# Optimization experiments

Measured on AMD Instinct MI355X. Metric: run time of the kernel, lower is better.

## Reference

```python
import jax, jax.numpy as jnp
import numpy as np
import math

N_EMBD = 1024
HIDDEN = 4 * N_EMBD
N_EXPERTS = 8
TOP_K = 2
B, T = 4, 2048


def new_gelu(x):
    c = math.sqrt(2.0 / math.pi)
    return 0.5 * x * (1.0 + jnp.tanh(c * (x + 0.044715 * x * x * x)))


def setup_inputs() -> dict:
    key = jax.random.key(0)
    ks = jax.random.split(key, 10)
    s = 0.02
    return {
        "x": jax.random.normal(ks[0], (B, T, N_EMBD), dtype=jnp.float32),
        # shared expert (1 shared expert)
        "Wfc_s": jax.random.normal(ks[1], (N_EMBD, HIDDEN), dtype=jnp.float32) * s,
        "bfc_s": jnp.zeros((HIDDEN,), dtype=jnp.float32),
        "Wproj_s": jax.random.normal(ks[2], (HIDDEN, N_EMBD), dtype=jnp.float32) * s,
        "bproj_s": jnp.zeros((N_EMBD,), dtype=jnp.float32),
        # router (no bias)
        "Wr": jax.random.normal(ks[3], (N_EMBD, N_EXPERTS), dtype=jnp.float32) * s,
        # routed experts, stacked on leading expert dim
        "Wfc": jax.random.normal(ks[4], (N_EXPERTS, N_EMBD, HIDDEN), dtype=jnp.float32) * s,
        "bfc": jnp.zeros((N_EXPERTS, HIDDEN), dtype=jnp.float32),
        "Wproj": jax.random.normal(ks[5], (N_EXPERTS, HIDDEN, N_EMBD), dtype=jnp.float32) * s,
        "bproj": jnp.zeros((N_EXPERTS, N_EMBD), dtype=jnp.float32),
    }


def _moe_forward(x, Wfc_s, bfc_s, Wproj_s, bproj_s, Wr, Wfc, bfc, Wproj, bproj):
    Bb, Tt, C = x.shape
    xf = x.reshape(Bb * Tt, C)  # [N, C]
    N = Bb * Tt

    # shared path (1 shared expert, divided by count == 1)
    shared = new_gelu(xf @ Wfc_s + bfc_s) @ Wproj_s + bproj_s

    # router
    logits = xf @ Wr                              # [N, E]
    probs = jax.nn.softmax(logits, axis=-1)
    topk_p, topk_i = jax.lax.top_k(probs, TOP_K)  # [N, K]
    topk_p = topk_p / jnp.sum(topk_p, axis=-1, keepdims=True)

    # dense combine weights: gate[n, e] = normalized prob if expert e selected else 0
    gate = jnp.zeros((N, N_EXPERTS), dtype=xf.dtype)
    gate = gate.at[jnp.arange(N)[:, None], topk_i].add(topk_p)

    routed = jnp.zeros_like(xf)
    for e in range(N_EXPERTS):  # small fixed loop over experts
        h = new_gelu(xf @ Wfc[e] + bfc[e]) @ Wproj[e] + bproj[e]
        routed = routed + h * gate[:, e:e + 1]

    return (shared + routed).reshape(Bb, Tt, C)


def reference(x, Wfc_s, bfc_s, Wproj_s, bproj_s, Wr, Wfc, bfc, Wproj, bproj):
    return _moe_forward(x, Wfc_s, bfc_s, Wproj_s, bproj_s, Wr, Wfc, bfc, Wproj, bproj)
```

## Files before the change

### kernel.cpp

```cpp
#include <hip/hip_runtime.h>
#include <stdint.h>

#define N_TOK 8192
#define C_DIM 1024
#define H_DIM 4096

typedef __bf16 bf16x8 __attribute__((ext_vector_type(8)));
typedef float floatx4 __attribute__((ext_vector_type(4)));

__device__ __forceinline__ short f2b(float f) {
    unsigned u = __float_as_uint(f);
    unsigned r = (u + 0x7FFFu + ((u >> 16) & 1u)) >> 16;
    return (short)(r & 0xFFFFu);
}

__device__ __forceinline__ float gelu_fast(float x) {
    const float a1 = -2.302114597830384f;
    const float a3 = -0.10294096656926834f;
    float x2 = x * x;
    float m = x * (a1 + a3 * x2);
    float e = __builtin_amdgcn_exp2f(m);
    return x * __builtin_amdgcn_rcpf(1.0f + e);
}

__device__ __forceinline__ void gl_lds16(const short* g, short* l) {
    __builtin_amdgcn_global_load_lds(
        (const __attribute__((address_space(1))) unsigned int*)g,
        (__attribute__((address_space(3))) unsigned int*)l, 16, 0, 0);
}

__global__ void cast_x_k(const float* __restrict__ in, short* __restrict__ out) {
    int i = (blockIdx.x * 256 + threadIdx.x) * 4;
    float4 v = *(const float4*)(in + i);
    short4 o;
    o.x = f2b(v.x); o.y = f2b(v.y); o.z = f2b(v.z); o.w = f2b(v.w);
    *(short4*)(out + i) = o;
}

__global__ void transpose_cast_k(const float* __restrict__ W, short* __restrict__ WT,
                                 int K, int N) {
    __shared__ float tile[32][33];
    size_t moff = (size_t)blockIdx.z * (size_t)K * (size_t)N;
    int n0 = blockIdx.x * 32, k0 = blockIdx.y * 32;
    int tx = threadIdx.x, ty = threadIdx.y;
#pragma unroll
    for (int j = 0; j < 32; j += 8)
        tile[ty + j][tx] = W[moff + (size_t)(k0 + ty + j) * N + n0 + tx];
    __syncthreads();
#pragma unroll
    for (int j = 0; j < 32; j += 8)
        WT[moff + (size_t)(n0 + ty + j) * K + k0 + tx] = f2b(tile[tx][ty + j]);
}

__global__ void init_shared_k(int* __restrict__ tok_list, float* __restrict__ gate_list,
                              int* __restrict__ counts) {
    int i = blockIdx.x * 256 + threadIdx.x;
    tok_list[8 * N_TOK + i] = i;
    gate_list[8 * N_TOK + i] = 1.0f;
    if (i == 0) counts[8] = N_TOK;
}

__global__ void router_k(const float* __restrict__ x, const float* __restrict__ Wr,
                         int* __restrict__ counts, int* __restrict__ tok_list,
                         float* __restrict__ gate_list, int* __restrict__ ent) {
    int token = blockIdx.x * 4 + (threadIdx.x >> 6);
    int lane = threadIdx.x & 63;
    const float* xr = x + (size_t)token * C_DIM;
    float p[8];
#pragma unroll
    for (int e = 0; e < 8; ++e) p[e] = 0.f;
    for (int jj = 0; jj < 4; ++jj) {
        int c = (jj * 64 + lane) * 4;
        float4 xv = *(const float4*)(xr + c);
        const float* w = Wr + (size_t)c * 8;
        float xs[4] = {xv.x, xv.y, xv.z, xv.w};
#pragma unroll
        for (int q = 0; q < 4; ++q)
#pragma unroll
            for (int e = 0; e < 8; ++e) p[e] += xs[q] * w[q * 8 + e];
    }
#pragma unroll
    for (int e = 0; e < 8; ++e)
#pragma unroll
        for (int off = 32; off > 0; off >>= 1) p[e] += __shfl_down(p[e], off);
    if (lane == 0) {
        float mx = p[0];
#pragma unroll
        for (int e = 1; e < 8; ++e) mx = fmaxf(mx, p[e]);
        float ex[8];
#pragma unroll
        for (int e = 0; e < 8; ++e) ex[e] = __expf(p[e] - mx);
        int i1 = 0;
#pragma unroll
        for (int e = 1; e < 8; ++e) if (ex[e] > ex[i1]) i1 = e;
        int i2 = (i1 == 0) ? 1 : 0;
#pragma unroll
        for (int e = 0; e < 8; ++e) if (e != i1 && ex[e] > ex[i2]) i2 = e;
        float s2 = ex[i1] + ex[i2];
        float g1 = ex[i1] / s2, g2 = ex[i2] / s2;
        int pos1 = atomicAdd(&counts[i1], 1);
        tok_list[i1 * N_TOK + pos1] = token;
        gate_list[i1 * N_TOK + pos1] = g1;
        ent[token * 2] = (i1 << 16) | pos1;
        int pos2 = atomicAdd(&counts[i2], 1);
        tok_list[i2 * N_TOK + pos2] = token;
        gate_list[i2 * N_TOK + pos2] = g2;
        ent[token * 2 + 1] = (i2 << 16) | pos2;
    }
}

__global__ void offsets_k(const int* __restrict__ counts, int* __restrict__ offs) {
    if (threadIdx.x == 0) {
        int a = 0;
        for (int e = 0; e < 9; ++e) { offs[e] = a; a += counts[e]; }
    }
}

#define SWZ(r) (((r) ^ ((r) >> 2)) & 3)

template <bool STAGE>
__device__ __forceinline__ void tile_body(
    char* cb, char* sb, int wave,
    const short* a0, const short* a1, const short* b0, const short* b1, int ko,
    const int (&aoff)[8], const int (&boff)[4], floatx4 (&acc)[8][4]) {
    bf16x8 afr[4], bfr[4];
#pragma unroll
    for (int n = 0; n < 4; ++n) bfr[n] = *(const bf16x8*)(cb + 32768 + boff[n]);
#pragma unroll
    for (int m = 0; m < 4; ++m) afr[m] = *(const bf16x8*)(cb + aoff[m]);
    if (STAGE) {
        gl_lds16(a0 + ko, (short*)(sb + wave * 1024));
        gl_lds16(a1 + ko, (short*)(sb + 8192 + wave * 1024));
    }
    __builtin_amdgcn_s_barrier();
    asm volatile("s_waitcnt lgkmcnt(0)" ::: "memory");
    __builtin_amdgcn_s_setprio(1);
#pragma unroll
    for (int m = 0; m < 4; ++m)
#pragma unroll
        for (int n = 0; n < 4; ++n)
            acc[m][n] = __builtin_amdgcn_mfma_f32_16x16x32_bf16(afr[m], bfr[n], acc[m][n], 0, 0, 0);
    __builtin_amdgcn_s_setprio(0);
    __builtin_amdgcn_s_barrier();
#pragma unroll
    for (int m = 0; m < 4; ++m) afr[m] = *(const bf16x8*)(cb + aoff[4 + m]);
    if (STAGE) {
        gl_lds16(b0 + ko, (short*)(sb + 32768 + wave * 1024));
        gl_lds16(b1 + ko, (short*)(sb + 40960 + wave * 1024));
    }
    __builtin_amdgcn_s_barrier();
    asm volatile("s_waitcnt lgkmcnt(0)" ::: "memory");
    __builtin_amdgcn_s_setprio(1);
#pragma unroll
    for (int m = 0; m < 4; ++m)
#pragma unroll
        for (int n = 0; n < 4; ++n)
            acc[4 + m][n] = __builtin_amdgcn_mfma_f32_16x16x32_bf16(afr[m], bfr[n], acc[4 + m][n], 0, 0, 0);
    __builtin_amdgcn_s_setprio(0);
    if (STAGE) asm volatile("s_waitcnt vmcnt(4)\n\ts_barrier" ::: "memory");
    else       asm volatile("s_waitcnt vmcnt(0)\n\ts_barrier" ::: "memory");
#pragma unroll
    for (int n = 0; n < 4; ++n) bfr[n] = *(const bf16x8*)(cb + 49152 + boff[n]);
#pragma unroll
    for (int m = 0; m < 4; ++m) afr[m] = *(const bf16x8*)(cb + 16384 + aoff[m]);
    if (STAGE) {
        gl_lds16(a0 + ko + 32, (short*)(sb + 16384 + wave * 1024));
        gl_lds16(a1 + ko + 32, (short*)(sb + 24576 + wave * 1024));
    }
    __builtin_amdgcn_s_barrier();
    asm volatile("s_waitcnt lgkmcnt(0)" ::: "memory");
    __builtin_amdgcn_s_setprio(1);
#pragma unroll
    for (int m = 0; m < 4; ++m)
#pragma unroll
        for (int n = 0; n < 4; ++n)
            acc[m][n] = __builtin_amdgcn_mfma_f32_16x16x32_bf16(afr[m], bfr[n], acc[m][n], 0, 0, 0);
    __builtin_amdgcn_s_setprio(0);
    __builtin_amdgcn_s_barrier();
#pragma unroll
    for (int m = 0; m < 4; ++m) afr[m] = *(const bf16x8*)(cb + 16384 + aoff[4 + m]);
    if (STAGE) {
        gl_lds16(b0 + ko + 32, (short*)(sb + 49152 + wave * 1024));
        gl_lds16(b1 + ko + 32, (short*)(sb + 57344 + wave * 1024));
    }
    __builtin_amdgcn_s_barrier();
    asm volatile("s_waitcnt lgkmcnt(0)" ::: "memory");
    __builtin_amdgcn_s_setprio(1);
#pragma unroll
    for (int m = 0; m < 4; ++m)
#pragma unroll
        for (int n = 0; n < 4; ++n)
            acc[4 + m][n] = __builtin_amdgcn_mfma_f32_16x16x32_bf16(afr[m], bfr[n], acc[4 + m][n], 0, 0, 0);
    __builtin_amdgcn_s_setprio(0);
    if (STAGE) asm volatile("s_waitcnt vmcnt(4)\n\ts_barrier" ::: "memory");
    else       __builtin_amdgcn_s_barrier();
}

template <bool IS_FC>
__global__ __launch_bounds__(512, 2) void gemm_k(
    const short* __restrict__ Abase, const short* __restrict__ Bbase,
    const float* __restrict__ biasbase, short* __restrict__ Out,
    const int* __restrict__ counts, const int* __restrict__ offs,
    const int* __restrict__ tok_base, const float* __restrict__ gate_base,
    int K, int N) {
    __shared__ __align__(16) char sm_b[131072];
    const int e = blockIdx.z;
    const int count = counts[e];
    const int mt = blockIdx.y, nt = blockIdx.x;
    if (mt * 256 >= count) return;
    const int off = offs[e];
    const int m0 = mt * 256, n0 = nt * 256;
    const short* Bm = Bbase + (size_t)e * (size_t)K * (size_t)N;
    const float* bias = biasbase + (size_t)e * (size_t)N;
    const int tid = threadIdx.x;
    const int wave = tid >> 6, lane = tid & 63;
    const int wm128 = (wave >> 2) * 128, wn64 = (wave & 3) * 64;
    const int fr = lane & 15, quad = lane >> 4;

    const int rs0 = wave * 16 + (lane >> 2), rs1 = 128 + rs0;
    const int ca0 = ((lane & 3) ^ SWZ(rs0)) * 8;
    const int ca1 = ((lane & 3) ^ SWZ(rs1)) * 8;
    int am0 = min(m0 + rs0, count - 1), am1 = min(m0 + rs1, count - 1);
    size_t ga0, ga1;
    if (IS_FC) {
        const int* list = tok_base + e * N_TOK;
        ga0 = (size_t)list[am0];
        ga1 = (size_t)list[am1];
    } else {
        ga0 = (size_t)(off + am0);
        ga1 = (size_t)(off + am1);
    }
    const short* a0 = Abase + ga0 * K + ca0;
    const short* a1 = Abase + ga1 * K + ca1;
    const short* b0 = Bm + (size_t)(n0 + rs0) * K + ca0;
    const short* b1 = Bm + (size_t)(n0 + rs1) * K + ca1;

    int aoff[8], boff[4];
#pragma unroll
    for (int m = 0; m < 8; ++m) {
        int r = wm128 + m * 16 + fr;
        aoff[m] = r * 64 + ((quad ^ SWZ(r)) << 4);
    }
#pragma unroll
    for (int n = 0; n < 4; ++n) {
        int r = wn64 + n * 16 + fr;
        boff[n] = r * 64 + ((quad ^ SWZ(r)) << 4);
    }

    floatx4 acc[8][4];
#pragma unroll
    for (int i = 0; i < 8; ++i)
#pragma unroll
        for (int j = 0; j < 4; ++j) acc[i][j] = (floatx4){0.f, 0.f, 0.f, 0.f};

    gl_lds16(a0,      (short*)(sm_b +     0 + wave * 1024));
    gl_lds16(a1,      (short*)(sm_b +  8192 + wave * 1024));
    gl_lds16(b0,      (short*)(sm_b + 32768 + wave * 1024));
    gl_lds16(b1,      (short*)(sm_b + 40960 + wave * 1024));
    gl_lds16(a0 + 32, (short*)(sm_b + 16384 + wave * 1024));
    gl_lds16(a1 + 32, (short*)(sm_b + 24576 + wave * 1024));
    gl_lds16(b0 + 32, (short*)(sm_b + 49152 + wave * 1024));
    gl_lds16(b1 + 32, (short*)(sm_b + 57344 + wave * 1024));
    asm volatile("s_waitcnt vmcnt(4)\n\ts_barrier" ::: "memory");

    const int kIters = K / 64;
    for (int t = 0; t < kIters - 1; ++t) {
        char* cb = sm_b + (t & 1) * 65536;
        char* sb = sm_b + ((t & 1) ^ 1) * 65536;
        tile_body<true>(cb, sb, wave, a0, a1, b0, b1, (t + 1) * 64, aoff, boff, acc);
    }
    tile_body<false>(sm_b + ((kIters - 1) & 1) * 65536, sm_b, wave,
                     a0, a1, b0, b1, 0, aoff, boff, acc);

    float bcol[4];
#pragma unroll
    for (int j = 0; j < 4; ++j) bcol[j] = bias[n0 + wn64 + j * 16 + fr];

    short* slab = (short*)sm_b + wave * 1152;
    const int rr = lane >> 2, cc = lane & 3;
    const int srow_m = m0 + wm128 + rr;
    short* sw = slab + quad * 288 + fr;
    const short* srd = slab + rr * 72 + cc * 16;
    const float* gl = gate_base + (IS_FC ? 0 : e * N_TOK);

#pragma unroll
    for (int i = 0; i < 8; ++i) {
        float g4[4];
        if (!IS_FC) {
#pragma unroll
            for (int r = 0; r < 4; ++r)
                g4[r] = gl[min(m0 + wm128 + i * 16 + quad * 4 + r, count - 1)];
        }
#pragma unroll
        for (int j = 0; j < 4; ++j)
#pragma unroll
            for (int r = 0; r < 4; ++r) {
                float v = acc[i][j][r] + bcol[j];
                if (IS_FC) v = gelu_fast(v); else v *= g4[r];
                sw[r * 72 + j * 16] = f2b(v);
            }
        int m = srow_m + i * 16;
        if (m < count) {
            int4 v0 = *(const int4*)srd;
            int4 v1 = *(const int4*)(srd + 8);
            short* orow = Out + (size_t)(off + m) * (size_t)N + n0 + wn64 + cc * 16;
            *(int4*)orow = v0;
            *(int4*)(orow + 8) = v1;
        }
        asm volatile("s_waitcnt lgkmcnt(0)" ::: "memory");
    }
}

__global__ void combine_k(float* __restrict__ out, const short* __restrict__ routc,
                          const int* __restrict__ ent, const int* __restrict__ offs) {
    int tid = threadIdx.x;
    int t = blockIdx.x * 2 + (tid >> 7);
    int c = (tid & 127) * 8;
    int p0 = ent[t * 2], p1 = ent[t * 2 + 1];
    size_t r0 = (size_t)(offs[p0 >> 16] + (p0 & 0xFFFF)) * 1024 + c;
    size_t r1 = (size_t)(offs[p1 >> 16] + (p1 & 0xFFFF)) * 1024 + c;
    size_t rs = (size_t)(16384 + t) * 1024 + c;
    int4 va = *(const int4*)(routc + rs);
    int4 vb = *(const int4*)(routc + r0);
    int4 vc = *(const int4*)(routc + r1);
    float o[8];
    const int* pa = (const int*)&va;
    const int* pb = (const int*)&vb;
    const int* pc = (const int*)&vc;
#pragma unroll
    for (int q = 0; q < 4; ++q) {
        unsigned a = pa[q], b = pb[q], cw = pc[q];
        o[2 * q] = __uint_as_float(a << 16) + __uint_as_float(b << 16) + __uint_as_float(cw << 16);
        o[2 * q + 1] = __uint_as_float(a & 0xFFFF0000u) + __uint_as_float(b & 0xFFFF0000u) +
                       __uint_as_float(cw & 0xFFFF0000u);
    }
    float* op = out + (size_t)t * 1024 + c;
    *(float4*)op = (float4){o[0], o[1], o[2], o[3]};
    *(float4*)(op + 4) = (float4){o[4], o[5], o[6], o[7]};
}

extern "C" void kernel_launch(void* const* d_in, const int* in_sizes, int n_in,
                              void* d_out, int out_size, void* d_ws, size_t ws_size,
                              hipStream_t stream) {
    const float* x       = (const float*)d_in[0];
    const float* Wfc_s   = (const float*)d_in[1];
    const float* bfc_s   = (const float*)d_in[2];
    const float* Wproj_s = (const float*)d_in[3];
    const float* bproj_s = (const float*)d_in[4];
    const float* Wr      = (const float*)d_in[5];
    const float* Wfc     = (const float*)d_in[6];
    const float* bfc     = (const float*)d_in[7];
    const float* Wproj   = (const float*)d_in[8];
    const float* bproj   = (const float*)d_in[9];
    float* out = (float*)d_out;

    char* p = (char*)d_ws;
    short* xb      = (short*)p; p += (size_t)N_TOK * C_DIM * 2;
    short* WfcT    = (short*)p; p += (size_t)9 * C_DIM * H_DIM * 2;
    short* WprojT  = (short*)p; p += (size_t)9 * C_DIM * H_DIM * 2;
    float* bfc_all = (float*)p; p += (size_t)9 * H_DIM * 4;
    float* bpj_all = (float*)p; p += (size_t)9 * C_DIM * 4;
    short* h       = (short*)p; p += (size_t)24576 * H_DIM * 2;
    short* routc   = (short*)p; p += (size_t)24576 * C_DIM * 2;
    int*   counts  = (int*)p;   p += 128;
    int*   offs    = (int*)p;   p += 128;
    int*   tok_list  = (int*)p;   p += (size_t)9 * N_TOK * 4;
    float* gate_list = (float*)p; p += (size_t)9 * N_TOK * 4;
    int*   ent     = (int*)p;   p += (size_t)N_TOK * 2 * 4;

    hipMemsetAsync(counts, 0, 64, stream);
    cast_x_k<<<8192, 256, 0, stream>>>(x, xb);
    transpose_cast_k<<<dim3(128, 32, 8), dim3(32, 8), 0, stream>>>(Wfc, WfcT, 1024, 4096);
    transpose_cast_k<<<dim3(128, 32, 1), dim3(32, 8), 0, stream>>>(Wfc_s, WfcT + (size_t)8 * C_DIM * H_DIM, 1024, 4096);
    transpose_cast_k<<<dim3(32, 128, 8), dim3(32, 8), 0, stream>>>(Wproj, WprojT, 4096, 1024);
    transpose_cast_k<<<dim3(32, 128, 1), dim3(32, 8), 0, stream>>>(Wproj_s, WprojT + (size_t)8 * C_DIM * H_DIM, 4096, 1024);
    hipMemcpyAsync(bfc_all, bfc, (size_t)8 * H_DIM * 4, hipMemcpyDeviceToDevice, stream);
    hipMemcpyAsync(bfc_all + 8 * H_DIM, bfc_s, (size_t)H_DIM * 4, hipMemcpyDeviceToDevice, stream);
    hipMemcpyAsync(bpj_all, bproj, (size_t)8 * C_DIM * 4, hipMemcpyDeviceToDevice, stream);
    hipMemcpyAsync(bpj_all + 8 * C_DIM, bproj_s, (size_t)C_DIM * 4, hipMemcpyDeviceToDevice, stream);
    init_shared_k<<<32, 256, 0, stream>>>(tok_list, gate_list, counts);
    router_k<<<2048, 256, 0, stream>>>(x, Wr, counts, tok_list, gate_list, ent);
    offsets_k<<<1, 64, 0, stream>>>(counts, offs);

    gemm_k<true><<<dim3(16, 32, 9), 512, 0, stream>>>(
        xb, WfcT, bfc_all, h, counts, offs, tok_list, gate_list, C_DIM, H_DIM);
    gemm_k<false><<<dim3(4, 32, 9), 512, 0, stream>>>(
        h, WprojT, bpj_all, routc, counts, offs, tok_list, gate_list, H_DIM, C_DIM);
    combine_k<<<4096, 256, 0, stream>>>(out, routc, ent, offs);
}
```

Baseline: 1.084 ms.

## Add 128-row tile variant for proj GEMM and swizzle block order

Templates the grouped GEMM on the M fragment count and adds a 128x256 tile body used for the down-projection GEMM. With N=1024 the earlier 256x256 tiles gave few blocks, so halving BM doubles the grid to improve CU occupancy and wave balance, and halves LDS use per block. It also remaps block ids with an 8-way swizzle so neighbouring blocks share B/A tiles in L2. Smaller tiles lower arithmetic intensity per block and re-read weights more often.

Result: slower. 1.322 ms (+21.9%).

```diff
diff --git a/kernel.cpp b/kernel.cpp
--- a/kernel.cpp
+++ b/kernel.cpp
@@ -119,7 +119,7 @@
 #define SWZ(r) (((r) ^ ((r) >> 2)) & 3)
 
 template <bool STAGE>
-__device__ __forceinline__ void tile_body(
+__device__ __forceinline__ void tile_body8(
     char* cb, char* sb, int wave,
     const short* a0, const short* a1, const short* b0, const short* b1, int ko,
     const int (&aoff)[8], const int (&boff)[4], floatx4 (&acc)[8][4]) {
@@ -196,49 +196,104 @@
     else       __builtin_amdgcn_s_barrier();
 }
 
-template <bool IS_FC>
+template <bool STAGE>
+__device__ __forceinline__ void tile_body4(
+    char* cb, char* sb, int wave,
+    const short* a0, const short* b0, const short* b1, int ko,
+    const int (&aoff)[4], const int (&boff)[4], floatx4 (&acc)[4][4]) {
+    bf16x8 afr[4], bfr[4];
+#pragma unroll
+    for (int n = 0; n < 4; ++n) bfr[n] = *(const bf16x8*)(cb + 16384 + boff[n]);
+#pragma unroll
+    for (int m = 0; m < 4; ++m) afr[m] = *(const bf16x8*)(cb + aoff[m]);
+    if (STAGE) {
+        gl_lds16(a0 + ko, (short*)(sb + wave * 1024));
+        gl_lds16(b0 + ko, (short*)(sb + 16384 + wave * 1024));
+        gl_lds16(b1 + ko, (short*)(sb + 24576 + wave * 1024));
+    }
+    __builtin_amdgcn_s_barrier();
+    asm volatile("s_waitcnt lgkmcnt(0)" ::: "memory");
+    __builtin_amdgcn_s_setprio(1);
+#pragma unroll
+    for (int m = 0; m < 4; ++m)
+#pragma unroll
+        for (int n = 0; n < 4; ++n)
+            acc[m][n] = __builtin_amdgcn_mfma_f32_16x16x32_bf16(afr[m], bfr[n], acc[m][n], 0, 0, 0);
+    __builtin_amdgcn_s_setprio(0);
+    if (STAGE) asm volatile("s_waitcnt vmcnt(3)\n\ts_barrier" ::: "memory");
+    else       asm volatile("s_waitcnt vmcnt(0)\n\ts_barrier" ::: "memory");
+#pragma unroll
+    for (int n = 0; n < 4; ++n) bfr[n] = *(const bf16x8*)(cb + 32768 + boff[n]);
+#pragma unroll
+    for (int m = 0; m < 4; ++m) afr[m] = *(const bf16x8*)(cb + 8192 + aoff[m]);
+    if (STAGE) {
+        gl_lds16(a0 + ko + 32, (short*)(sb + 8192 + wave * 1024));
+        gl_lds16(b0 + ko + 32, (short*)(sb + 32768 + wave * 1024));
+        gl_lds16(b1 + ko + 32, (short*)(sb + 40960 + wave * 1024));
+    }
+    __builtin_amdgcn_s_barrier();
+    asm volatile("s_waitcnt lgkmcnt(0)" ::: "memory");
+    __builtin_amdgcn_s_setprio(1);
+#pragma unroll
+    for (int m = 0; m < 4; ++m)
+#pragma unroll
+        for (int n = 0; n < 4; ++n)
+            acc[m][n] = __builtin_amdgcn_mfma_f32_16x16x32_bf16(afr[m], bfr[n], acc[m][n], 0, 0, 0);
+    __builtin_amdgcn_s_setprio(0);
+    if (STAGE) asm volatile("s_waitcnt vmcnt(3)\n\ts_barrier" ::: "memory");
+    else       __builtin_amdgcn_s_barrier();
+}
+
+template <bool IS_FC, int MF>
 __global__ __launch_bounds__(512, 2) void gemm_k(
     const short* __restrict__ Abase, const short* __restrict__ Bbase,
     const float* __restrict__ biasbase, short* __restrict__ Out,
     const int* __restrict__ counts, const int* __restrict__ offs,
     const int* __restrict__ tok_base, const float* __restrict__ gate_base,
     int K, int N) {
-    __shared__ __align__(16) char sm_b[131072];
+    constexpr int BM = MF * 32;
+    constexpr int APLANE = BM * 64;
+    constexpr int BUFB = 2 * APLANE + 32768;
+    __shared__ __align__(16) char sm_b[2 * BUFB];
     const int e = blockIdx.z;
     const int count = counts[e];
-    const int mt = blockIdx.y, nt = blockIdx.x;
-    if (mt * 256 >= count) return;
+    const int gx = gridDim.x, gy = gridDim.y;
+    const int bid = blockIdx.y * gx + blockIdx.x;
+    const int cpx = (gx * gy) >> 3;
+    const int swz = (bid & 7) * cpx + (bid >> 3);
+    const int mt = swz % gy, nt = swz / gy;
+    if (mt * BM >= count) return;
     const int off = offs[e];
-    const int m0 = mt * 256, n0 = nt * 256;
+    const int m0 = mt * BM, n0 = nt * 256;
     const short* Bm = Bbase + (size_t)e * (size_t)K * (size_t)N;
     const float* bias = biasbase + (size_t)e * (size_t)N;
     const int tid = threadIdx.x;
     const int wave = tid >> 6, lane = tid & 63;
-    const int wm128 = (wave >> 2) * 128, wn64 = (wave & 3) * 64;
+    const int wmM = (wave >> 2) * (MF * 16), wn64 = (wave & 3) * 64;
     const int fr = lane & 15, quad = lane >> 4;
 
     const int rs0 = wave * 16 + (lane >> 2), rs1 = 128 + rs0;
     const int ca0 = ((lane & 3) ^ SWZ(rs0)) * 8;
     const int ca1 = ((lane & 3) ^ SWZ(rs1)) * 8;
-    int am0 = min(m0 + rs0, count - 1), am1 = min(m0 + rs1, count - 1);
-    size_t ga0, ga1;
+    int am0 = min(m0 + rs0, count - 1);
+    size_t ga0, ga1 = 0;
     if (IS_FC) {
         const int* list = tok_base + e * N_TOK;
         ga0 = (size_t)list[am0];
-        ga1 = (size_t)list[am1];
+        if (MF == 8) ga1 = (size_t)list[min(m0 + rs1, count - 1)];
     } else {
         ga0 = (size_t)(off + am0);
-        ga1 = (size_t)(off + am1);
+        if (MF == 8) ga1 = (size_t)(off + min(m0 + rs1, count - 1));
     }
     const short* a0 = Abase + ga0 * K + ca0;
     const short* a1 = Abase + ga1 * K + ca1;
     const short* b0 = Bm + (size_t)(n0 + rs0) * K + ca0;
     const short* b1 = Bm + (size_t)(n0 + rs1) * K + ca1;
 
-    int aoff[8], boff[4];
-#pragma unroll
-    for (int m = 0; m < 8; ++m) {
-        int r = wm128 + m * 16 + fr;
+    int aoff[MF], boff[4];
+#pragma unroll
+    for (int m = 0; m < MF; ++m) {
+        int r = wmM + m * 16 + fr;
         aoff[m] = r * 64 + ((quad ^ SWZ(r)) << 4);
     }
 #pragma unroll
@@ -247,30 +302,50 @@
         boff[n] = r * 64 + ((quad ^ SWZ(r)) << 4);
     }
 
-    floatx4 acc[8][4];
-#pragma unroll
-    for (int i = 0; i < 8; ++i)
+    floatx4 acc[MF][4];
+#pragma unroll
+    for (int i = 0; i < MF; ++i)
 #pragma unroll
         for (int j = 0; j < 4; ++j) acc[i][j] = (floatx4){0.f, 0.f, 0.f, 0.f};
 
-    gl_lds16(a0,      (short*)(sm_b +     0 + wave * 1024));
-    gl_lds16(a1,      (short*)(sm_b +  8192 + wave * 1024));
-    gl_lds16(b0,      (short*)(sm_b + 32768 + wave * 1024));
-    gl_lds16(b1,      (short*)(sm_b + 40960 + wave * 1024));
-    gl_lds16(a0 + 32, (short*)(sm_b + 16384 + wave * 1024));
-    gl_lds16(a1 + 32, (short*)(sm_b + 24576 + wave * 1024));
-    gl_lds16(b0 + 32, (short*)(sm_b + 49152 + wave * 1024));
-    gl_lds16(b1 + 32, (short*)(sm_b + 57344 + wave * 1024));
-    asm volatile("s_waitcnt vmcnt(4)\n\ts_barrier" ::: "memory");
-
     const int kIters = K / 64;
-    for (int t = 0; t < kIters - 1; ++t) {
-        char* cb = sm_b + (t & 1) * 65536;
-        char* sb = sm_b + ((t & 1) ^ 1) * 65536;
-        tile_body<true>(cb, sb, wave, a0, a1, b0, b1, (t + 1) * 64, aoff, boff, acc);
-    }
-    tile_body<false>(sm_b + ((kIters - 1) & 1) * 65536, sm_b, wave,
-                     a0, a1, b0, b1, 0, aoff, boff, acc);
+    if (MF == 8) {
+        gl_lds16(a0,      (short*)(sm_b +     0 + wave * 1024));
+        gl_lds16(a1,      (short*)(sm_b +  8192 + wave * 1024));
+        gl_lds16(b0,      (short*)(sm_b + 32768 + wave * 1024));
+        gl_lds16(b1,      (short*)(sm_b + 40960 + wave * 1024));
+        gl_lds16(a0 + 32, (short*)(sm_b + 16384 + wave * 1024));
+        gl_lds16(a1 + 32, (short*)(sm_b + 24576 + wave * 1024));
+        gl_lds16(b0 + 32, (short*)(sm_b + 49152 + wave * 1024));
+        gl_lds16(b1 + 32, (short*)(sm_b + 57344 + wave * 1024));
+        asm volatile("s_waitcnt vmcnt(4)\n\ts_barrier" ::: "memory");
+        for (int t = 0; t < kIters - 1; ++t) {
+            char* cb = sm_b + (t & 1) * BUFB;
+            char* sb = sm_b + ((t & 1) ^ 1) * BUFB;
+            tile_body8<true>(cb, sb, wave, a0, a1, b0, b1, (t + 1) * 64,
+                             (const int(&)[8])aoff, boff, (floatx4(&)[8][4])acc);
+        }
+        tile_body8<false>(sm_b + ((kIters - 1) & 1) * BUFB, sm_b,
+                          wave, a0, a1, b0, b1, 0,
+                          (const int(&)[8])aoff, boff, (floatx4(&)[8][4])acc);
+    } else {
+        gl_lds16(a0,      (short*)(sm_b +     0 + wave * 1024));
+        gl_lds16(b0,      (short*)(sm_b + 16384 + wave * 1024));
+        gl_lds16(b1,      (short*)(sm_b + 24576 + wave * 1024));
+        gl_lds16(a0 + 32, (short*)(sm_b +  8192 + wave * 1024));
+        gl_lds16(b0 + 32, (short*)(sm_b + 32768 + wave * 1024));
+        gl_lds16(b1 + 32, (short*)(sm_b + 40960 + wave * 1024));
+        asm volatile("s_waitcnt vmcnt(3)\n\ts_barrier" ::: "memory");
+        for (int t = 0; t < kIters - 1; ++t) {
+            char* cb = sm_b + (t & 1) * BUFB;
+            char* sb = sm_b + ((t & 1) ^ 1) * BUFB;
+            tile_body4<true>(cb, sb, wave, a0, b0, b1, (t + 1) * 64,
+                             (const int(&)[4])aoff, boff, (floatx4(&)[4][4])acc);
+        }
+        tile_body4<false>(sm_b + ((kIters - 1) & 1) * BUFB, sm_b,
+                          wave, a0, b0, b1, 0,
+                          (const int(&)[4])aoff, boff, (floatx4(&)[4][4])acc);
+    }
 
     float bcol[4];
 #pragma unroll
@@ -278,18 +353,18 @@
 
     short* slab = (short*)sm_b + wave * 1152;
     const int rr = lane >> 2, cc = lane & 3;
-    const int srow_m = m0 + wm128 + rr;
+    const int srow_m = m0 + wmM + rr;
     short* sw = slab + quad * 288 + fr;
     const short* srd = slab + rr * 72 + cc * 16;
     const float* gl = gate_base + (IS_FC ? 0 : e * N_TOK);
 
 #pragma unroll
-    for (int i = 0; i < 8; ++i) {
+    for (int i = 0; i < MF; ++i) {
         float g4[4];
         if (!IS_FC) {
 #pragma unroll
             for (int r = 0; r < 4; ++r)
-                g4[r] = gl[min(m0 + wm128 + i * 16 + quad * 4 + r, count - 1)];
+                g4[r] = gl[min(m0 + wmM + i * 16 + quad * 4 + r, count - 1)];
         }
 #pragma unroll
         for (int j = 0; j < 4; ++j)
@@ -382,9 +457,9 @@
     router_k<<<2048, 256, 0, stream>>>(x, Wr, counts, tok_list, gate_list, ent);
     offsets_k<<<1, 64, 0, stream>>>(counts, offs);
 
-    gemm_k<true><<<dim3(16, 32, 9), 512, 0, stream>>>(
+    gemm_k<true, 8><<<dim3(16, 32, 9), 512, 0, stream>>>(
         xb, WfcT, bfc_all, h, counts, offs, tok_list, gate_list, C_DIM, H_DIM);
-    gemm_k<false><<<dim3(4, 32, 9), 512, 0, stream>>>(
+    gemm_k<false, 4><<<dim3(4, 64, 9), 512, 0, stream>>>(
         h, WprojT, bpj_all, routc, counts, offs, tok_list, gate_list, H_DIM, C_DIM);
     combine_k<<<4096, 256, 0, stream>>>(out, routc, ent, offs);
 }
```

## Restructure GEMM LDS tile layout to full 64-wide rows and vectorize weight transpose

Applied to the files above, without the earlier changes.

The GEMM LDS staging changes from two 32-column k-halves per tile to one row-major layout with 128-byte rows (64 bf16) and an XOR swizzle over 8 chunks. All eight global-to-LDS loads for the next k-tile are now issued at the start of each tile body, and the second k-half is read via an XOR-64 offset. The pipeline now waits with vmcnt(0) instead of keeping four loads in flight. Separately, the weight transpose-cast kernel uses float4 loads and short4 stores with an 8x32 thread block, aiming for more efficient memory access during weight preprocessing.

New measurement: 1.122 ms. +3.5%, slower.

```diff
diff --git a/kernel.cpp b/kernel.cpp
--- a/kernel.cpp
+++ b/kernel.cpp
@@ -43,13 +43,18 @@
     size_t moff = (size_t)blockIdx.z * (size_t)K * (size_t)N;
     int n0 = blockIdx.x * 32, k0 = blockIdx.y * 32;
     int tx = threadIdx.x, ty = threadIdx.y;
-#pragma unroll
-    for (int j = 0; j < 32; j += 8)
-        tile[ty + j][tx] = W[moff + (size_t)(k0 + ty + j) * N + n0 + tx];
+    float4 v = *(const float4*)(W + moff + (size_t)(k0 + ty) * N + n0 + tx * 4);
+    tile[ty][tx * 4 + 0] = v.x;
+    tile[ty][tx * 4 + 1] = v.y;
+    tile[ty][tx * 4 + 2] = v.z;
+    tile[ty][tx * 4 + 3] = v.w;
     __syncthreads();
-#pragma unroll
-    for (int j = 0; j < 32; j += 8)
-        WT[moff + (size_t)(n0 + ty + j) * K + k0 + tx] = f2b(tile[tx][ty + j]);
+    short4 o;
+    o.x = f2b(tile[tx * 4 + 0][ty]);
+    o.y = f2b(tile[tx * 4 + 1][ty]);
+    o.z = f2b(tile[tx * 4 + 2][ty]);
+    o.w = f2b(tile[tx * 4 + 3][ty]);
+    *(short4*)(WT + moff + (size_t)(n0 + ty) * K + k0 + tx * 4) = o;
 }
 
 __global__ void init_shared_k(int* __restrict__ tok_list, float* __restrict__ gate_list,
@@ -116,12 +121,11 @@
     }
 }
 
-#define SWZ(r) (((r) ^ ((r) >> 2)) & 3)
-
 template <bool STAGE>
 __device__ __forceinline__ void tile_body(
     char* cb, char* sb, int wave,
-    const short* a0, const short* a1, const short* b0, const short* b1, int ko,
+    const short* a0, const short* a1, const short* a2, const short* a3,
+    const short* b0, const short* b1, const short* b2, const short* b3, int ko,
     const int (&aoff)[8], const int (&boff)[4], floatx4 (&acc)[8][4]) {
     bf16x8 afr[4], bfr[4];
 #pragma unroll
@@ -129,8 +133,14 @@
 #pragma unroll
     for (int m = 0; m < 4; ++m) afr[m] = *(const bf16x8*)(cb + aoff[m]);
     if (STAGE) {
-        gl_lds16(a0 + ko, (short*)(sb + wave * 1024));
-        gl_lds16(a1 + ko, (short*)(sb + 8192 + wave * 1024));
+        gl_lds16(a0 + ko, (short*)(sb +     0 + wave * 1024));
+        gl_lds16(a1 + ko, (short*)(sb +  8192 + wave * 1024));
+        gl_lds16(a2 + ko, (short*)(sb + 16384 + wave * 1024));
+        gl_lds16(a3 + ko, (short*)(sb + 24576 + wave * 1024));
+        gl_lds16(b0 + ko, (short*)(sb + 32768 + wave * 1024));
+        gl_lds16(b1 + ko, (short*)(sb + 40960 + wave * 1024));
+        gl_lds16(b2 + ko, (short*)(sb + 49152 + wave * 1024));
+        gl_lds16(b3 + ko, (short*)(sb + 57344 + wave * 1024));
     }
     __builtin_amdgcn_s_barrier();
     asm volatile("s_waitcnt lgkmcnt(0)" ::: "memory");
@@ -144,10 +154,6 @@
     __builtin_amdgcn_s_barrier();
 #pragma unroll
     for (int m = 0; m < 4; ++m) afr[m] = *(const bf16x8*)(cb + aoff[4 + m]);
-    if (STAGE) {
-        gl_lds16(b0 + ko, (short*)(sb + 32768 + wave * 1024));
-        gl_lds16(b1 + ko, (short*)(sb + 40960 + wave * 1024));
-    }
     __builtin_amdgcn_s_barrier();
     asm volatile("s_waitcnt lgkmcnt(0)" ::: "memory");
     __builtin_amdgcn_s_setprio(1);
@@ -157,16 +163,11 @@
         for (int n = 0; n < 4; ++n)
             acc[4 + m][n] = __builtin_amdgcn_mfma_f32_16x16x32_bf16(afr[m], bfr[n], acc[4 + m][n], 0, 0, 0);
     __builtin_amdgcn_s_setprio(0);
-    if (STAGE) asm volatile("s_waitcnt vmcnt(4)\n\ts_barrier" ::: "memory");
-    else       asm volatile("s_waitcnt vmcnt(0)\n\ts_barrier" ::: "memory");
-#pragma unroll
-    for (int n = 0; n < 4; ++n) bfr[n] = *(const bf16x8*)(cb + 49152 + boff[n]);
-#pragma unroll
-    for (int m = 0; m < 4; ++m) afr[m] = *(const bf16x8*)(cb + 16384 + aoff[m]);
-    if (STAGE) {
-        gl_lds16(a0 + ko + 32, (short*)(sb + 16384 + wave * 1024));
-        gl_lds16(a1 + ko + 32, (short*)(sb + 24576 + wave * 1024));
-    }
+    __builtin_amdgcn_s_barrier();
+#pragma unroll
+    for (int n = 0; n < 4; ++n) bfr[n] = *(const bf16x8*)(cb + 32768 + (boff[n] ^ 64));
+#pragma unroll
+    for (int m = 0; m < 4; ++m) afr[m] = *(const bf16x8*)(cb + (aoff[m] ^ 64));
     __builtin_amdgcn_s_barrier();
     asm volatile("s_waitcnt lgkmcnt(0)" ::: "memory");
     __builtin_amdgcn_s_setprio(1);
@@ -178,11 +179,7 @@
     __builtin_amdgcn_s_setprio(0);
     __builtin_amdgcn_s_barrier();
 #pragma unroll
-    for (int m = 0; m < 4; ++m) afr[m] = *(const bf16x8*)(cb + 16384 + aoff[4 + m]);
-    if (STAGE) {
-        gl_lds16(b0 + ko + 32, (short*)(sb + 49152 + wave * 1024));
-        gl_lds16(b1 + ko + 32, (short*)(sb + 57344 + wave * 1024));
-    }
+    for (int m = 0; m < 4; ++m) afr[m] = *(const bf16x8*)(cb + (aoff[4 + m] ^ 64));
     __builtin_amdgcn_s_barrier();
     asm volatile("s_waitcnt lgkmcnt(0)" ::: "memory");
     __builtin_amdgcn_s_setprio(1);
@@ -192,7 +189,7 @@
         for (int n = 0; n < 4; ++n)
             acc[4 + m][n] = __builtin_amdgcn_mfma_f32_16x16x32_bf16(afr[m], bfr[n], acc[4 + m][n], 0, 0, 0);
     __builtin_amdgcn_s_setprio(0);
-    if (STAGE) asm volatile("s_waitcnt vmcnt(4)\n\ts_barrier" ::: "memory");
+    if (STAGE) asm volatile("s_waitcnt vmcnt(0)\n\ts_barrier" ::: "memory");
     else       __builtin_amdgcn_s_barrier();
 }
 
@@ -217,34 +214,30 @@
     const int wm128 = (wave >> 2) * 128, wn64 = (wave & 3) * 64;
     const int fr = lane & 15, quad = lane >> 4;
 
-    const int rs0 = wave * 16 + (lane >> 2), rs1 = 128 + rs0;
-    const int ca0 = ((lane & 3) ^ SWZ(rs0)) * 8;
-    const int ca1 = ((lane & 3) ^ SWZ(rs1)) * 8;
-    int am0 = min(m0 + rs0, count - 1), am1 = min(m0 + rs1, count - 1);
-    size_t ga0, ga1;
-    if (IS_FC) {
+    const int l8 = lane >> 3;
+    const int kb = (lane & 7) ^ l8;
+    const short *ap[4], *bp[4];
+    {
         const int* list = tok_base + e * N_TOK;
-        ga0 = (size_t)list[am0];
-        ga1 = (size_t)list[am1];
-    } else {
-        ga0 = (size_t)(off + am0);
-        ga1 = (size_t)(off + am1);
-    }
-    const short* a0 = Abase + ga0 * K + ca0;
-    const short* a1 = Abase + ga1 * K + ca1;
-    const short* b0 = Bm + (size_t)(n0 + rs0) * K + ca0;
-    const short* b1 = Bm + (size_t)(n0 + rs1) * K + ca1;
+#pragma unroll
+        for (int j = 0; j < 4; ++j) {
+            int rm = min(m0 + j * 64 + wave * 8 + l8, count - 1);
+            size_t ga = IS_FC ? (size_t)list[rm] : (size_t)(off + rm);
+            ap[j] = Abase + ga * K + kb * 8;
+            bp[j] = Bm + (size_t)(n0 + j * 64 + wave * 8 + l8) * K + kb * 8;
+        }
+    }
 
     int aoff[8], boff[4];
 #pragma unroll
     for (int m = 0; m < 8; ++m) {
         int r = wm128 + m * 16 + fr;
-        aoff[m] = r * 64 + ((quad ^ SWZ(r)) << 4);
+        aoff[m] = r * 128 + ((quad ^ (r & 7)) << 4);
     }
 #pragma unroll
     for (int n = 0; n < 4; ++n) {
         int r = wn64 + n * 16 + fr;
-        boff[n] = r * 64 + ((quad ^ SWZ(r)) << 4);
+        boff[n] = r * 128 + ((quad ^ (r & 7)) << 4);
     }
 
     floatx4 acc[8][4];
@@ -253,24 +246,26 @@
 #pragma unroll
         for (int j = 0; j < 4; ++j) acc[i][j] = (floatx4){0.f, 0.f, 0.f, 0.f};
 
-    gl_lds16(a0,      (short*)(sm_b +     0 + wave * 1024));
-    gl_lds16(a1,      (short*)(sm_b +  8192 + wave * 1024));
-    gl_lds16(b0,      (short*)(sm_b + 32768 + wave * 1024));
-    gl_lds16(b1,      (short*)(sm_b + 40960 + wave * 1024));
-    gl_lds16(a0 + 32, (short*)(sm_b + 16384 + wave * 1024));
-    gl_lds16(a1 + 32, (short*)(sm_b + 24576 + wave * 1024));
-    gl_lds16(b0 + 32, (short*)(sm_b + 49152 + wave * 1024));
-    gl_lds16(b1 + 32, (short*)(sm_b + 57344 + wave * 1024));
-    asm volatile("s_waitcnt vmcnt(4)\n\ts_barrier" ::: "memory");
+    gl_lds16(ap[0], (short*)(sm_b +     0 + wave * 1024));
+    gl_lds16(ap[1], (short*)(sm_b +  8192 + wave * 1024));
+    gl_lds16(ap[2], (short*)(sm_b + 16384 + wave * 1024));
+    gl_lds16(ap[3], (short*)(sm_b + 24576 + wave * 1024));
+    gl_lds16(bp[0], (short*)(sm_b + 32768 + wave * 1024));
+    gl_lds16(bp[1], (short*)(sm_b + 40960 + wave * 1024));
+    gl_lds16(bp[2], (short*)(sm_b + 49152 + wave * 1024));
+    gl_lds16(bp[3], (short*)(sm_b + 57344 + wave * 1024));
+    asm volatile("s_waitcnt vmcnt(0)\n\ts_barrier" ::: "memory");
 
     const int kIters = K / 64;
     for (int t = 0; t < kIters - 1; ++t) {
         char* cb = sm_b + (t & 1) * 65536;
         char* sb = sm_b + ((t & 1) ^ 1) * 65536;
-        tile_body<true>(cb, sb, wave, a0, a1, b0, b1, (t + 1) * 64, aoff, boff, acc);
+        tile_body<true>(cb, sb, wave, ap[0], ap[1], ap[2], ap[3],
+                        bp[0], bp[1], bp[2], bp[3], (t + 1) * 64, aoff, boff, acc);
     }
     tile_body<false>(sm_b + ((kIters - 1) & 1) * 65536, sm_b, wave,
-                     a0, a1, b0, b1, 0, aoff, boff, acc);
+                     ap[0], ap[1], ap[2], ap[3], bp[0], bp[1], bp[2], bp[3], 0,
+                     aoff, boff, acc);
 
     float bcol[4];
 #pragma unroll
@@ -370,10 +365,10 @@
 
     hipMemsetAsync(counts, 0, 64, stream);
     cast_x_k<<<8192, 256, 0, stream>>>(x, xb);
-    transpose_cast_k<<<dim3(128, 32, 8), dim3(32, 8), 0, stream>>>(Wfc, WfcT, 1024, 4096);
-    transpose_cast_k<<<dim3(128, 32, 1), dim3(32, 8), 0, stream>>>(Wfc_s, WfcT + (size_t)8 * C_DIM * H_DIM, 1024, 4096);
-    transpose_cast_k<<<dim3(32, 128, 8), dim3(32, 8), 0, stream>>>(Wproj, WprojT, 4096, 1024);
-    transpose_cast_k<<<dim3(32, 128, 1), dim3(32, 8), 0, stream>>>(Wproj_s, WprojT + (size_t)8 * C_DIM * H_DIM, 4096, 1024);
+    transpose_cast_k<<<dim3(128, 32, 8), dim3(8, 32), 0, stream>>>(Wfc, WfcT, 1024, 4096);
+    transpose_cast_k<<<dim3(128, 32, 1), dim3(8, 32), 0, stream>>>(Wfc_s, WfcT + (size_t)8 * C_DIM * H_DIM, 1024, 4096);
+    transpose_cast_k<<<dim3(32, 128, 8), dim3(8, 32), 0, stream>>>(Wproj, WprojT, 4096, 1024);
+    transpose_cast_k<<<dim3(32, 128, 1), dim3(8, 32), 0, stream>>>(Wproj_s, WprojT + (size_t)8 * C_DIM * H_DIM, 4096, 1024);
     hipMemcpyAsync(bfc_all, bfc, (size_t)8 * H_DIM * 4, hipMemcpyDeviceToDevice, stream);
     hipMemcpyAsync(bfc_all + 8 * H_DIM, bfc_s, (size_t)H_DIM * 4, hipMemcpyDeviceToDevice, stream);
     hipMemcpyAsync(bpj_all, bproj, (size_t)8 * C_DIM * 4, hipMemcpyDeviceToDevice, stream);
```
